# Optimization experiments

Measured on AMD Instinct MI355X. Metric: run time of the kernel, lower is better.

The kernel has to match this reference:

```python
import jax, jax.numpy as jnp
import numpy as np

N_NODES = 100000
N_EDGES = 1600000
SZ_IN = 128
DIM_I = 1024


def setup_inputs() -> dict:
    key = jax.random.key(0)
    k1, k2, k3, k4, k5 = jax.random.split(key, 5)
    x = jax.random.normal(k1, (N_NODES, SZ_IN), dtype=jnp.float32)
    edge_index = jax.random.randint(k2, (2, N_EDGES), 0, N_NODES, dtype=jnp.int64)
    # torch Linear weight is [out_features, in_features]
    agg_W = jax.random.normal(k3, (SZ_IN, SZ_IN), dtype=jnp.float32) / np.sqrt(SZ_IN)
    agg_b = jnp.zeros((SZ_IN,), dtype=jnp.float32)
    lin_W = jax.random.normal(k4, (DIM_I, 2 * SZ_IN), dtype=jnp.float32) / np.sqrt(2 * SZ_IN)
    return {"x": x, "edge_index": edge_index, "agg_W": agg_W, "agg_b": agg_b, "lin_W": lin_W}


def reference(x, edge_index, agg_W, agg_b, lin_W):
    # GraphSAGE layer, depth=1, agg='max', concat=True, training mode (no self-loop/dropout edits).
    u, v = edge_index[0], edge_index[1]
    n = x.shape[0]
    # gather neighbor features, linear + ReLU  -> [E, sz_in]
    msg = jax.nn.relu(x[v] @ agg_W.T + agg_b)
    # scatter-max per target node; torch_scatter initializes out to zeros,
    # so missing nodes get 0 and all results are max(values, 0)
    hn = jnp.maximum(jax.ops.segment_max(msg, u, num_segments=n), 0.0)
    # concat + linear (no bias) + ReLU -> [N, dim_i]
    h = jax.nn.relu(jnp.concatenate([x, hn], axis=1) @ lin_W.T)
    return h
```

## Files before the change

### kernel.cpp

```cpp
#include <hip/hip_runtime.h>
#include <hip/hip_bf16.h>

typedef __attribute__((ext_vector_type(8))) short short8;
typedef __attribute__((ext_vector_type(4))) float f32x4;

__device__ __forceinline__ float bfu2f(unsigned short u) {
    unsigned int x = ((unsigned int)u) << 16;
    float f;
    __builtin_memcpy(&f, &x, 4);
    return f;
}
__device__ __forceinline__ unsigned short f2bfu(float f) {
    unsigned int x;
    __builtin_memcpy(&x, &f, 4);
    unsigned int r = (x + 0x7FFFu + ((x >> 16) & 1u)) >> 16;
    return (unsigned short)r;
}

__device__ __forceinline__ void gload_lds16(const void* g, void* l) {
    __builtin_amdgcn_global_load_lds(
        (const __attribute__((address_space(1))) void*)g,
        (__attribute__((address_space(3))) void*)l, 16, 0, 0);
}

#define BM 128
#define BN 128
#define BK 32
#define LDA 32

template<bool F32OUT>
__global__ __launch_bounds__(256, 2)
void gemm_bt(const unsigned short* __restrict__ Alo,
             const unsigned short* __restrict__ Ahi,
             const unsigned short* __restrict__ B,
             const float* __restrict__ bias,
             void* __restrict__ Cv,
             int M, int N, int K, int relu)
{
    __shared__ unsigned short As[BM * LDA];
    __shared__ unsigned short Bs[BN * LDA];

    const int tid  = threadIdx.x;
    const int nwg  = gridDim.x * gridDim.y;
    int lid = blockIdx.y * gridDim.x + blockIdx.x;
    int wg  = lid;
    if ((nwg & 7) == 0) {
        int cpx = nwg >> 3;
        wg = (lid & 7) * cpx + (lid >> 3);
    }
    const int m0 = (wg / gridDim.x) * BM;
    const int n0 = (wg % gridDim.x) * BN;

    const int lane = tid & 63;
    const int wave = tid >> 6;
    const int wr   = wave >> 1;
    const int wc   = wave & 1;
    const int fm   = lane & 15;
    const int fq   = lane >> 4;

    f32x4 acc[4][4] = {};

    const int wbase = tid & ~63;

    for (int k0 = 0; k0 < K; k0 += BK) {
        __syncthreads();
        const unsigned short* Ab = (k0 < 128) ? Alo : Ahi;
        const int ka = (k0 < 128) ? k0 : (k0 - 128);
        #pragma unroll
        for (int i = 0; i < 2; ++i) {
            int c  = i * 256 + tid;
            int r  = c >> 2;
            int c8 = (c & 3) << 3;
            int grow = m0 + r;
            if (grow >= M) grow = M - 1;
            gload_lds16(Ab + (size_t)grow * 128 + ka + c8,
                        &As[(i * 256 + wbase) * 8]);
            gload_lds16(B + (size_t)(n0 + r) * K + k0 + c8,
                        &Bs[(i * 256 + wbase) * 8]);
        }
        __syncthreads();

        short8 af[4], bf[4];
        #pragma unroll
        for (int i = 0; i < 4; ++i)
            af[i] = *(const short8*)(&As[(wr * 64 + i * 16 + fm) * LDA + fq * 8]);
        #pragma unroll
        for (int j = 0; j < 4; ++j)
            bf[j] = *(const short8*)(&Bs[(wc * 64 + j * 16 + fm) * LDA + fq * 8]);

        #pragma unroll
        for (int i = 0; i < 4; ++i)
            #pragma unroll
            for (int j = 0; j < 4; ++j)
                acc[i][j] = __builtin_amdgcn_mfma_f32_16x16x32_bf16(
                                af[i], bf[j], acc[i][j], 0, 0, 0);
    }

    #pragma unroll
    for (int i = 0; i < 4; ++i) {
        #pragma unroll
        for (int r = 0; r < 4; ++r) {
            int gm = m0 + wr * 64 + i * 16 + fq * 4 + r;
            if (gm < M) {
                #pragma unroll
                for (int j = 0; j < 4; ++j) {
                    int gn = n0 + wc * 64 + j * 16 + fm;
                    float val = acc[i][j][r];
                    if (bias) val += bias[gn];
                    if (relu) val = fmaxf(val, 0.0f);
                    if (F32OUT)
                        __builtin_nontemporal_store(val,
                            &((float*)Cv)[(size_t)gm * N + gn]);
                    else
                        ((unsigned short*)Cv)[(size_t)gm * N + gn] = f2bfu(val);
                }
            }
        }
    }
}

__device__ __forceinline__ void cvt4(const float* __restrict__ src,
                                     unsigned short* __restrict__ dst, int t)
{
    float4 f = ((const float4*)src)[t];
    ushort4 o;
    o.x = f2bfu(f.x); o.y = f2bfu(f.y); o.z = f2bfu(f.z); o.w = f2bfu(f.w);
    ((ushort4*)dst)[t] = o;
}

__global__ __launch_bounds__(256)
void prep_k(const float* __restrict__ x, unsigned short* __restrict__ xb, int n4x,
            const float* __restrict__ aW, unsigned short* __restrict__ awb, int n4a,
            const float* __restrict__ lW, unsigned short* __restrict__ lwb, int n4l,
            int* __restrict__ deg, int n4d)
{
    int t = blockIdx.x * 256 + threadIdx.x;
    if (t < n4x) { cvt4(x, xb, t); return; }
    t -= n4x;
    if (t < n4a) { cvt4(aW, awb, t); return; }
    t -= n4a;
    if (t < n4l) { cvt4(lW, lwb, t); return; }
    t -= n4l;
    if (t < n4d) ((int4*)deg)[t] = make_int4(0, 0, 0, 0);
}

__global__ __launch_bounds__(256)
void deg_k(const int* __restrict__ ei, int* __restrict__ deg, int E)
{
    int e = (blockIdx.x * 256 + threadIdx.x) * 4;
    if (e >= E) return;
    if (e + 3 < E) {
        int4 u = *(const int4*)(ei + e);
        atomicAdd(&deg[u.x], 1);
        atomicAdd(&deg[u.y], 1);
        atomicAdd(&deg[u.z], 1);
        atomicAdd(&deg[u.w], 1);
    } else {
        for (int j = 0; j < 4 && e + j < E; ++j) atomicAdd(&deg[ei[e + j]], 1);
    }
}

__global__ __launch_bounds__(256)
void scan1_k(const int* __restrict__ deg, int* __restrict__ bsum, int NN)
{
    __shared__ int s[256];
    int t = threadIdx.x;
    int base = blockIdx.x * 1024 + t * 4;
    int sum = 0;
    if (base + 3 < NN) {
        int4 d = *(const int4*)(deg + base);
        sum = d.x + d.y + d.z + d.w;
    } else {
        for (int j = 0; j < 4; ++j) if (base + j < NN) sum += deg[base + j];
    }
    s[t] = sum;
    __syncthreads();
    for (int ofs = 128; ofs > 0; ofs >>= 1) {
        if (t < ofs) s[t] += s[t + ofs];
        __syncthreads();
    }
    if (t == 0) bsum[blockIdx.x] = s[0];
}

__global__ __launch_bounds__(256)
void scan2_k(int* __restrict__ bsum, int* __restrict__ offN, int NB)
{
    __shared__ int s[256];
    int t = threadIdx.x;
    int v = (t < NB) ? bsum[t] : 0;
    s[t] = v;
    __syncthreads();
    for (int ofs = 1; ofs < 256; ofs <<= 1) {
        int w = (t >= ofs) ? s[t - ofs] : 0;
        __syncthreads();
        s[t] += w;
        __syncthreads();
    }
    if (t < NB) bsum[t] = (t > 0) ? s[t - 1] : 0;
    if (t == 255) *offN = s[255];
}

__global__ __launch_bounds__(256)
void scan3_k(const int* __restrict__ deg, const int* __restrict__ bsum,
             int* __restrict__ off, int* __restrict__ cur, int NN)
{
    __shared__ int s[256];
    int t = threadIdx.x;
    int base = blockIdx.x * 1024 + t * 4;
    int d0 = 0, d1 = 0, d2 = 0, d3 = 0;
    if (base + 3 < NN) {
        int4 d = *(const int4*)(deg + base);
        d0 = d.x; d1 = d.y; d2 = d.z; d3 = d.w;
    } else {
        if (base     < NN) d0 = deg[base];
        if (base + 1 < NN) d1 = deg[base + 1];
        if (base + 2 < NN) d2 = deg[base + 2];
        if (base + 3 < NN) d3 = deg[base + 3];
    }
    s[t] = d0 + d1 + d2 + d3;
    __syncthreads();
    for (int ofs = 1; ofs < 256; ofs <<= 1) {
        int w = (t >= ofs) ? s[t - ofs] : 0;
        __syncthreads();
        s[t] += w;
        __syncthreads();
    }
    int o0 = bsum[blockIdx.x] + ((t > 0) ? s[t - 1] : 0);
    int o1 = o0 + d0, o2 = o1 + d1, o3 = o2 + d2;
    if (base + 3 < NN) {
        *(int4*)(off + base) = make_int4(o0, o1, o2, o3);
        *(int4*)(cur + base) = make_int4(o0, o1, o2, o3);
    } else {
        if (base     < NN) { off[base]     = o0; cur[base]     = o0; }
        if (base + 1 < NN) { off[base + 1] = o1; cur[base + 1] = o1; }
        if (base + 2 < NN) { off[base + 2] = o2; cur[base + 2] = o2; }
        if (base + 3 < NN) { off[base + 3] = o3; cur[base + 3] = o3; }
    }
}

__global__ __launch_bounds__(256)
void fill_k(const int* __restrict__ ei, int* __restrict__ cur,
            int* __restrict__ adj, int E)
{
    int e = (blockIdx.x * 256 + threadIdx.x) * 4;
    if (e >= E) return;
    if (e + 3 < E) {
        int4 u = *(const int4*)(ei + e);
        int4 v = *(const int4*)(ei + E + e);
        int p0 = atomicAdd(&cur[u.x], 1); adj[p0] = v.x;
        int p1 = atomicAdd(&cur[u.y], 1); adj[p1] = v.y;
        int p2 = atomicAdd(&cur[u.z], 1); adj[p2] = v.z;
        int p3 = atomicAdd(&cur[u.w], 1); adj[p3] = v.w;
    } else {
        for (int j = 0; j < 4 && e + j < E; ++j) {
            int u = ei[e + j], v = ei[E + e + j];
            int p = atomicAdd(&cur[u], 1); adj[p] = v;
        }
    }
}

__global__ __launch_bounds__(256)
void gather_max_k(const int* __restrict__ off, const int* __restrict__ adj,
                  const unsigned short* __restrict__ y,
                  unsigned short* __restrict__ hnb, int NN)
{
    int t = blockIdx.x * 256 + threadIdx.x;
    int u = t >> 4;
    if (u >= NN) return;
    int c = (t & 15) << 3;
    const unsigned short* yc = y + c;
    int s = off[u], e2 = off[u + 1];
    short8 a0 = {0, 0, 0, 0, 0, 0, 0, 0};
    short8 a1 = {0, 0, 0, 0, 0, 0, 0, 0};
    int i = s;
    for (; i + 3 < e2; i += 4) {
        int v0 = adj[i], v1 = adj[i + 1], v2 = adj[i + 2], v3 = adj[i + 3];
        short8 y0 = *(const short8*)(yc + (size_t)v0 * 128);
        short8 y1 = *(const short8*)(yc + (size_t)v1 * 128);
        short8 y2 = *(const short8*)(yc + (size_t)v2 * 128);
        short8 y3 = *(const short8*)(yc + (size_t)v3 * 128);
        a0 = __builtin_elementwise_max(a0, y0);
        a1 = __builtin_elementwise_max(a1, y1);
        a0 = __builtin_elementwise_max(a0, y2);
        a1 = __builtin_elementwise_max(a1, y3);
    }
    for (; i < e2; ++i) {
        short8 y0 = *(const short8*)(yc + (size_t)adj[i] * 128);
        a0 = __builtin_elementwise_max(a0, y0);
    }
    a0 = __builtin_elementwise_max(a0, a1);
    *(short8*)(hnb + (size_t)u * 128 + c) = a0;
}

extern "C" void kernel_launch(void* const* d_in, const int* in_sizes, int n_in,
                              void* d_out, int out_size, void* d_ws, size_t ws_size,
                              hipStream_t stream)
{
    const float* x     = (const float*)d_in[0];
    const int*   ei    = (const int*)d_in[1];
    const float* agg_W = (const float*)d_in[2];
    const float* agg_b = (const float*)d_in[3];
    const float* lin_W = (const float*)d_in[4];
    float*       out   = (float*)d_out;

    const int NN = in_sizes[0] / 128;
    const int E  = in_sizes[1] / 2;
    const int DI = in_sizes[4] / 256;

    char* ws = (char*)d_ws;
    const size_t xN = (size_t)NN * 128;
    unsigned short* xb  = (unsigned short*)ws;
    unsigned short* y   = xb + xN;
    unsigned short* hnb = y + xN;
    unsigned short* awb = hnb + xN;
    unsigned short* lwb = awb + 128 * 128;
    char* p = (char*)(lwb + (size_t)DI * 256);
    int* deg = (int*)p;
    int* off = deg + NN;
    int* cur = off + NN + 1;
    int* adj = cur + NN;
    int* bsum = adj + E;

    const int MT = (NN + BM - 1) / BM;
    const int NB = (NN + 1023) / 1024;

    const int n4x = (int)(xN / 4);
    const int n4a = 128 * 128 / 4;
    const int n4l = DI * 256 / 4;
    const int n4d = (NN + 3) / 4;
    {
        long long tot = (long long)n4x + n4a + n4l + n4d;
        prep_k<<<(int)((tot + 255) / 256), 256, 0, stream>>>(
            x, xb, n4x, agg_W, awb, n4a, lin_W, lwb, n4l, deg, n4d);
    }

    gemm_bt<false><<<dim3(1, MT), 256, 0, stream>>>(xb, xb, awb, agg_b, y, NN, 128, 128, 0);

    deg_k<<<(E / 4 + 255) / 256, 256, 0, stream>>>(ei, deg, E);
    scan1_k<<<NB, 256, 0, stream>>>(deg, bsum, NN);
    scan2_k<<<1, 256, 0, stream>>>(bsum, off + NN, NB);
    scan3_k<<<NB, 256, 0, stream>>>(deg, bsum, off, cur, NN);
    fill_k<<<(E / 4 + 255) / 256, 256, 0, stream>>>(ei, cur, adj, E);

    {
        long long threads = (long long)NN * 16;
        int blocks = (int)((threads + 255) / 256);
        gather_max_k<<<blocks, 256, 0, stream>>>(off, adj, y, hnb, NN);
    }

    gemm_bt<true><<<dim3(DI / BN, MT), 256, 0, stream>>>(xb, hnb, lwb, nullptr, out, NN, DI, 256, 1);
}
```

Before: 753.7 us.

## Fuse first GEMM with degree count and fold block-sum scan into scan3

```diff
diff --git a/kernel.cpp b/kernel.cpp
--- a/kernel.cpp
+++ b/kernel.cpp
@@ -29,28 +29,16 @@
 #define LDA 32
 
 template<bool F32OUT>
-__global__ __launch_bounds__(256, 2)
-void gemm_bt(const unsigned short* __restrict__ Alo,
-             const unsigned short* __restrict__ Ahi,
-             const unsigned short* __restrict__ B,
-             const float* __restrict__ bias,
-             void* __restrict__ Cv,
-             int M, int N, int K, int relu)
-{
-    __shared__ unsigned short As[BM * LDA];
-    __shared__ unsigned short Bs[BN * LDA];
-
+__device__ __forceinline__ void gemm_tile(
+    const unsigned short* __restrict__ Alo,
+    const unsigned short* __restrict__ Ahi,
+    const unsigned short* __restrict__ B,
+    const float* __restrict__ bias,
+    void* __restrict__ Cv,
+    int M, int N, int K, int relu, int m0, int n0,
+    unsigned short* As, unsigned short* Bs)
+{
     const int tid  = threadIdx.x;
-    const int nwg  = gridDim.x * gridDim.y;
-    int lid = blockIdx.y * gridDim.x + blockIdx.x;
-    int wg  = lid;
-    if ((nwg & 7) == 0) {
-        int cpx = nwg >> 3;
-        wg = (lid & 7) * cpx + (lid >> 3);
-    }
-    const int m0 = (wg / gridDim.x) * BM;
-    const int n0 = (wg % gridDim.x) * BN;
-
     const int lane = tid & 63;
     const int wave = tid >> 6;
     const int wr   = wave >> 1;
@@ -119,6 +107,58 @@
     }
 }
 
+template<bool F32OUT>
+__global__ __launch_bounds__(256, 2)
+void gemm_bt(const unsigned short* __restrict__ Alo,
+             const unsigned short* __restrict__ Ahi,
+             const unsigned short* __restrict__ B,
+             const float* __restrict__ bias,
+             void* __restrict__ Cv,
+             int M, int N, int K, int relu)
+{
+    __shared__ unsigned short As[BM * LDA];
+    __shared__ unsigned short Bs[BN * LDA];
+
+    const int nwg  = gridDim.x * gridDim.y;
+    int lid = blockIdx.y * gridDim.x + blockIdx.x;
+    int wg  = lid;
+    if ((nwg & 7) == 0) {
+        int cpx = nwg >> 3;
+        wg = (lid & 7) * cpx + (lid >> 3);
+    }
+    const int m0 = (wg / gridDim.x) * BM;
+    const int n0 = (wg % gridDim.x) * BN;
+    gemm_tile<F32OUT>(Alo, Ahi, B, bias, Cv, M, N, K, relu, m0, n0, As, Bs);
+}
+
+__global__ __launch_bounds__(256, 2)
+void gemm1_deg_k(const unsigned short* __restrict__ xb,
+                 const unsigned short* __restrict__ awb,
+                 const float* __restrict__ bias,
+                 unsigned short* __restrict__ y, int M, int MT,
+                 const int* __restrict__ ei, int* __restrict__ deg, int E)
+{
+    __shared__ unsigned short As[BM * LDA];
+    __shared__ unsigned short Bs[BN * LDA];
+
+    int b = blockIdx.x;
+    if (b < MT) {
+        gemm_tile<false>(xb, xb, awb, bias, y, M, 128, 128, 0, b * BM, 0, As, Bs);
+        return;
+    }
+    int e = ((b - MT) * 256 + (int)threadIdx.x) * 4;
+    if (e >= E) return;
+    if (e + 3 < E) {
+        int4 u = *(const int4*)(ei + e);
+        atomicAdd(&deg[u.x], 1);
+        atomicAdd(&deg[u.y], 1);
+        atomicAdd(&deg[u.z], 1);
+        atomicAdd(&deg[u.w], 1);
+    } else {
+        for (int j = 0; j < 4 && e + j < E; ++j) atomicAdd(&deg[ei[e + j]], 1);
+    }
+}
+
 __device__ __forceinline__ void cvt4(const float* __restrict__ src,
                                      unsigned short* __restrict__ dst, int t)
 {
@@ -145,22 +185,6 @@
 }
 
 __global__ __launch_bounds__(256)
-void deg_k(const int* __restrict__ ei, int* __restrict__ deg, int E)
-{
-    int e = (blockIdx.x * 256 + threadIdx.x) * 4;
-    if (e >= E) return;
-    if (e + 3 < E) {
-        int4 u = *(const int4*)(ei + e);
-        atomicAdd(&deg[u.x], 1);
-        atomicAdd(&deg[u.y], 1);
-        atomicAdd(&deg[u.z], 1);
-        atomicAdd(&deg[u.w], 1);
-    } else {
-        for (int j = 0; j < 4 && e + j < E; ++j) atomicAdd(&deg[ei[e + j]], 1);
-    }
-}
-
-__global__ __launch_bounds__(256)
 void scan1_k(const int* __restrict__ deg, int* __restrict__ bsum, int NN)
 {
     __shared__ int s[256];
@@ -183,29 +207,24 @@
 }
 
 __global__ __launch_bounds__(256)
-void scan2_k(int* __restrict__ bsum, int* __restrict__ offN, int NB)
-{
+void scan3_k(const int* __restrict__ deg, const int* __restrict__ bsum,
+             int* __restrict__ off, int* __restrict__ cur, int NN, int NB)
+{
+    __shared__ int sb[256];
     __shared__ int s[256];
     int t = threadIdx.x;
-    int v = (t < NB) ? bsum[t] : 0;
-    s[t] = v;
+
+    sb[t] = (t < NB) ? bsum[t] : 0;
     __syncthreads();
     for (int ofs = 1; ofs < 256; ofs <<= 1) {
-        int w = (t >= ofs) ? s[t - ofs] : 0;
-        __syncthreads();
-        s[t] += w;
-        __syncthreads();
-    }
-    if (t < NB) bsum[t] = (t > 0) ? s[t - 1] : 0;
-    if (t == 255) *offN = s[255];
-}
-
-__global__ __launch_bounds__(256)
-void scan3_k(const int* __restrict__ deg, const int* __restrict__ bsum,
-             int* __restrict__ off, int* __restrict__ cur, int NN)
-{
-    __shared__ int s[256];
-    int t = threadIdx.x;
+        int w = (t >= ofs) ? sb[t - ofs] : 0;
+        __syncthreads();
+        sb[t] += w;
+        __syncthreads();
+    }
+    int blkbase = (blockIdx.x > 0) ? sb[blockIdx.x - 1] : 0;
+    if (blockIdx.x == 0 && t == 255) off[NN] = sb[255];
+
     int base = blockIdx.x * 1024 + t * 4;
     int d0 = 0, d1 = 0, d2 = 0, d3 = 0;
     if (base + 3 < NN) {
@@ -225,7 +244,7 @@
         s[t] += w;
         __syncthreads();
     }
-    int o0 = bsum[blockIdx.x] + ((t > 0) ? s[t - 1] : 0);
+    int o0 = blkbase + ((t > 0) ? s[t - 1] : 0);
     int o1 = o0 + d0, o2 = o1 + d1, o3 = o2 + d2;
     if (base + 3 < NN) {
         *(int4*)(off + base) = make_int4(o0, o1, o2, o3);
@@ -323,6 +342,7 @@
 
     const int MT = (NN + BM - 1) / BM;
     const int NB = (NN + 1023) / 1024;
+    const int DB = (E / 4 + 255) / 256;
 
     const int n4x = (int)(xN / 4);
     const int n4a = 128 * 128 / 4;
@@ -334,12 +354,10 @@
             x, xb, n4x, agg_W, awb, n4a, lin_W, lwb, n4l, deg, n4d);
     }
 
-    gemm_bt<false><<<dim3(1, MT), 256, 0, stream>>>(xb, xb, awb, agg_b, y, NN, 128, 128, 0);
-
-    deg_k<<<(E / 4 + 255) / 256, 256, 0, stream>>>(ei, deg, E);
+    gemm1_deg_k<<<MT + DB, 256, 0, stream>>>(xb, awb, agg_b, y, NN, MT, ei, deg, E);
+
     scan1_k<<<NB, 256, 0, stream>>>(deg, bsum, NN);
-    scan2_k<<<1, 256, 0, stream>>>(bsum, off + NN, NB);
-    scan3_k<<<NB, 256, 0, stream>>>(deg, bsum, off, cur, NN);
+    scan3_k<<<NB, 256, 0, stream>>>(deg, bsum, off, cur, NN, NB);
     fill_k<<<(E / 4 + 255) / 256, 256, 0, stream>>>(ei, cur, adj, E);
 
     {
```

After: 734.6 us. -2.5%, faster.
